# Performance work log

Measured on AMD Instinct MI355X. Metric: run time of the kernel, lower is better.

## Reference

```python
import jax, jax.numpy as jnp
import numpy as np

N_IN = 1024
N_OUT = 1024
N_SAMPLES = 64
BATCH = 4096
SIGMA_INITIAL = 0.1
MUMAX_INITIAL = 1.0


def setup_inputs() -> dict:
    key = jax.random.key(0)
    ks = jax.random.split(key, 5)
    lsig = jnp.float32(np.log(SIGMA_INITIAL))
    return {
        "x": jax.random.normal(ks[0], (BATCH, N_IN), dtype=jnp.float32),
        "w_mu": jax.random.uniform(ks[1], (N_OUT, N_IN), dtype=jnp.float32,
                                   minval=-MUMAX_INITIAL, maxval=MUMAX_INITIAL),
        "w_lsigma": jnp.full((N_OUT, N_IN), lsig, dtype=jnp.float32),
        "b_mu": jax.random.uniform(ks[2], (N_OUT,), dtype=jnp.float32,
                                   minval=-MUMAX_INITIAL, maxval=MUMAX_INITIAL),
        "b_lsigma": jnp.full((N_OUT,), lsig, dtype=jnp.float32),
        "r1": jax.random.normal(ks[3], (N_SAMPLES, N_OUT, N_IN), dtype=jnp.float32),
        "r2": jax.random.normal(ks[4], (N_SAMPLES, N_OUT), dtype=jnp.float32),
        "N_samples": N_SAMPLES,
    }


def reference(x, w_mu, w_lsigma, b_mu, b_lsigma, r1, r2, N_samples):
    # Reparameterized weight/bias samples: (S, N_out, N_in), (S, N_out)
    w = w_mu + jnp.exp(w_lsigma) * r1
    b = b_mu + jnp.exp(b_lsigma) * r2
    # y[s, b, o] = sum_i x[b, i] * w[s, o, i] + b[s, o]
    y = jnp.einsum('bi,soi->sbo', x, w) + b[:, None, :]
    return y
```

## Files before the change

### kernel.cpp

```cpp
#include <hip/hip_runtime.h>
#include <hip/hip_bf16.h>
#include <hip/hip_fp8.h>
#include <stdint.h>
#include <type_traits>

#define NIN  1024
#define NOUT 1024
#define NB   4096

typedef float f32x4  __attribute__((ext_vector_type(4)));
typedef float f32x16 __attribute__((ext_vector_type(16)));
typedef __bf16 bf16x8 __attribute__((ext_vector_type(8)));
typedef int   i32x4 __attribute__((ext_vector_type(4)));
typedef int   i32x8 __attribute__((ext_vector_type(8)));

typedef const __attribute__((address_space(1))) unsigned int* gp1_t;
typedef __attribute__((address_space(3))) unsigned int* lp3_t;

__device__ __forceinline__ void gload16(const void* g, void* l) {
    __builtin_amdgcn_global_load_lds((gp1_t)g, (lp3_t)l, 16, 0, 0);
}

__device__ __forceinline__ unsigned short f2bf(float f) {
    __bf16 h = (__bf16)f;
    return __builtin_bit_cast(unsigned short, h);
}

__device__ __forceinline__ unsigned int pk4_fp8(float a, float b, float c, float d) {
#if __has_builtin(__builtin_amdgcn_cvt_pk_fp8_f32)
    int p = __builtin_amdgcn_cvt_pk_fp8_f32(a, b, 0, false);
    p = __builtin_amdgcn_cvt_pk_fp8_f32(c, d, p, true);
    return (unsigned int)p;
#else
    __hip_fp8_e4m3 qa(a), qb(b), qc(c), qd(d);
    return (unsigned int)qa.__x | ((unsigned int)qb.__x << 8) |
           ((unsigned int)qc.__x << 16) | ((unsigned int)qd.__x << 24);
#endif
}

#define BAR   __builtin_amdgcn_s_barrier()
#define LGK0  do { asm volatile("s_waitcnt lgkmcnt(0)" ::: "memory"); __builtin_amdgcn_sched_barrier(0); } while (0)
#define VMW2  do { asm volatile("s_waitcnt vmcnt(2)"  ::: "memory"); __builtin_amdgcn_sched_barrier(0); } while (0)
#define VMW0  do { asm volatile("s_waitcnt vmcnt(0)"  ::: "memory"); __builtin_amdgcn_sched_barrier(0); } while (0)

__global__ void cvt_x_kernel(const float* __restrict__ x, unsigned short* __restrict__ xb) {
    int i = blockIdx.x * blockDim.x + threadIdx.x;
    f32x4 v = reinterpret_cast<const f32x4*>(x)[i];
    ushort4 o;
    o.x = f2bf(v.x); o.y = f2bf(v.y); o.z = f2bf(v.z); o.w = f2bf(v.w);
    reinterpret_cast<ushort4*>(xb)[i] = o;
}

__global__ void cvt_x_fp8(const float* __restrict__ x, unsigned int* __restrict__ xf8) {
    int i = blockIdx.x * blockDim.x + threadIdx.x;
    f32x4 v = reinterpret_cast<const f32x4*>(x)[i];
    xf8[i] = pk4_fp8(v.x, v.y, v.z, v.w);
}

__global__ void cvt_r1_fp8(const float* __restrict__ wls, const float* __restrict__ r1,
                           unsigned int* __restrict__ rf8, int s0) {
    int idx = blockIdx.x * blockDim.x + threadIdx.x;
    int i4 = idx & 262143;
    int c  = idx >> 18;
    f32x4 ls = reinterpret_cast<const f32x4*>(wls)[i4];
    const f32x4* rp = reinterpret_cast<const f32x4*>(r1 + ((size_t)(s0 + c) << 20));
    f32x4 r = __builtin_nontemporal_load(rp + i4);
    rf8[idx] = pk4_fp8(__expf(ls.x) * r.x, __expf(ls.y) * r.y,
                       __expf(ls.z) * r.z, __expf(ls.w) * r.w);
}

__global__ void bias_kernel(const float* __restrict__ bmu, const float* __restrict__ bls,
                            const float* __restrict__ r2, float* __restrict__ bias, int total) {
    int i = blockIdx.x * blockDim.x + threadIdx.x;
    if (i < total) {
        int o = i & (NOUT - 1);
        bias[i] = bmu[o] + __expf(bls[o]) * r2[i];
    }
}

__launch_bounds__(512, 2)
__global__ void gemm256(const unsigned short* __restrict__ xb,
                        const unsigned short* __restrict__ wb,
                        float* __restrict__ out, int nwg) {
    __shared__ __align__(16) char smem[131072];
    const int tid = threadIdx.x;
    const int l   = tid & 63;
    const int w   = tid >> 6;
    const int wr  = w >> 2, wc = w & 3;

    const int b   = blockIdx.x;
    const int q8  = nwg >> 3;
    const int g   = (b & 7) * q8 + (b >> 3);
    const int mi  = g & 15;
    const int ni  = g >> 4;
    const int m0  = mi * 256;
    const int n0  = ni * 256;

    const int srow = l >> 3;
    const int scol = ((l & 7) ^ srow) * 8;
    const size_t slane = (size_t)srow * NIN + scol;

    const int rowp  = (l & 15) * 128;
    const int colp0 = ((l >> 4) ^ (l & 7)) << 4;

    f32x4 acc[8][4] = {};
    bf16x8 aF[4][2], b0F[2][2], b1F[2][2];

    const unsigned short* xbase = xb + (size_t)m0 * NIN;
    const unsigned short* wbase = wb + (size_t)n0 * NIN;

    auto STAGE = [&](int buf, int kt, int q) {
        const int R = (q & 3) * 64 + w * 8;
        const unsigned short* src = ((q < 4) ? xbase : wbase)
                                    + (size_t)R * NIN + kt * 64 + slane;
        char* dst = smem + buf * 65536 + ((q >= 4) ? 32768 : 0) + R * 128;
        gload16(src, dst);
    };
    auto LDA = [&](int buf, int mh) {
        const char* base = smem + buf * 65536 + (wr * 128 + mh * 64) * 128 + rowp;
        #pragma unroll
        for (int mb = 0; mb < 4; ++mb) {
            aF[mb][0] = *(const bf16x8*)(base + mb * 2048 + colp0);
            aF[mb][1] = *(const bf16x8*)(base + mb * 2048 + (colp0 ^ 64));
        }
    };
    auto LDB = [&](bf16x8 (&bF)[2][2], int buf, int nh) {
        const char* base = smem + buf * 65536 + 32768 + (wc * 64 + nh * 32) * 128 + rowp;
        #pragma unroll
        for (int nb = 0; nb < 2; ++nb) {
            bF[nb][0] = *(const bf16x8*)(base + nb * 2048 + colp0);
            bF[nb][1] = *(const bf16x8*)(base + nb * 2048 + (colp0 ^ 64));
        }
    };
    auto MM = [&](auto MHc, auto NHc, bf16x8 (&bF)[2][2]) {
        constexpr int MH = decltype(MHc)::value;
        constexpr int NH = decltype(NHc)::value;
        __builtin_amdgcn_s_setprio(1);
        #pragma unroll
        for (int mb = 0; mb < 4; ++mb)
            #pragma unroll
            for (int nb = 0; nb < 2; ++nb)
                #pragma unroll
                for (int kk = 0; kk < 2; ++kk)
                    acc[MH * 4 + mb][NH * 2 + nb] = __builtin_amdgcn_mfma_f32_16x16x32_bf16(
                        aF[mb][kk], bF[nb][kk], acc[MH * 4 + mb][NH * 2 + nb], 0, 0, 0);
        __builtin_amdgcn_s_setprio(0);
    };

    auto C0 = std::integral_constant<int, 0>{};
    auto C1 = std::integral_constant<int, 1>{};

    auto ITER = [&](auto LASTc, int t1, int t2, int t3) {
        constexpr bool LAST = decltype(LASTc)::value;
        LDA(0, 0); LDB(b0F, 0, 0);
        STAGE(1, t1, 2); STAGE(1, t1, 3);
        BAR; LGK0; MM(C0, C0, b0F); BAR;
        LDB(b1F, 0, 1);
        STAGE(1, t1, 4); STAGE(1, t1, 5);
        BAR; LGK0; MM(C0, C1, b1F); BAR;
        LDA(0, 1);
        STAGE(1, t1, 6); STAGE(1, t1, 7);
        BAR; LGK0; MM(C1, C1, b1F); BAR;
        if constexpr (!LAST) { STAGE(0, t2, 0); STAGE(0, t2, 1); }
        BAR; MM(C1, C0, b0F);
        if constexpr (LAST) { VMW0; } else { VMW2; }
        BAR;
        LDA(1, 0); LDB(b0F, 1, 0);
        if constexpr (!LAST) { STAGE(0, t2, 2); STAGE(0, t2, 3); }
        BAR; LGK0; MM(C0, C0, b0F); BAR;
        LDB(b1F, 1, 1);
        if constexpr (!LAST) { STAGE(0, t2, 4); STAGE(0, t2, 5); }
        BAR; LGK0; MM(C0, C1, b1F); BAR;
        LDA(1, 1);
        if constexpr (!LAST) { STAGE(0, t2, 6); STAGE(0, t2, 7); }
        BAR; LGK0; MM(C1, C1, b1F); BAR;
        if constexpr (!LAST) {
            STAGE(1, t3, 0); STAGE(1, t3, 1);
            BAR; MM(C1, C0, b0F); VMW2; BAR;
        } else {
            MM(C1, C0, b0F);
        }
    };

    #pragma unroll
    for (int q = 0; q < 8; ++q) STAGE(0, 0, q);
    STAGE(1, 1, 0); STAGE(1, 1, 1);
    VMW2; BAR;

    #pragma unroll 1
    for (int i = 0; i < 7; ++i)
        ITER(std::false_type{}, 2 * i + 1, 2 * i + 2, 2 * i + 3);
    ITER(std::true_type{}, 15, 16, 17);

    const int oc = n0 + wc * 64 + (l & 15);
    float* outp = out;
    #pragma unroll
    for (int mb = 0; mb < 8; ++mb) {
        #pragma unroll
        for (int i2 = 0; i2 < 4; ++i2) {
            int row = m0 + wr * 128 + mb * 16 + (l >> 4) * 4 + i2;
            float* rp = outp + (size_t)row * NOUT + oc;
            #pragma unroll
            for (int nb = 0; nb < 4; ++nb)
                rp[nb * 16] = acc[mb][nb][i2];
        }
    }
}

__launch_bounds__(512, 2)
__global__ void gemm256mx(const unsigned char* __restrict__ xf8,
                          const unsigned char* __restrict__ rf8,
                          const float* __restrict__ y0,
                          const float* __restrict__ bias,
                          float* __restrict__ out, int s0, int nwg) {
    __shared__ __align__(16) char smem[131072];
    const int tid = threadIdx.x;
    const int l   = tid & 63;
    const int w   = tid >> 6;
    const int wr  = w >> 2, wc = w & 3;

    const int b   = blockIdx.x;
    const int q8  = nwg >> 3;
    const int g   = (b & 7) * q8 + (b >> 3);
    const int mi  = g & 15;
    const int ni  = g >> 4;
    const int m0  = mi * 256;
    const int n0  = ni * 256;

    const int srow  = l >> 3;
    const int scolb = ((l & 7) ^ srow) * 16;
    const size_t slane = (size_t)srow * NIN + scolb;

    const int arow = l & 31;
    const int swz  = l & 7;
    const int kgrp = (l >> 5) * 2;

    f32x16 acc[4][2] = {};
    i32x8 aF[2][2], b0F[2], b1F[2];

    const unsigned char* xbase = xf8 + (size_t)m0 * NIN;
    const unsigned char* rbase = rf8 + (size_t)n0 * NIN;

    auto STAGE = [&](int buf, int kt, int q) {
        const int R = (q & 3) * 64 + w * 8;
        const unsigned char* src = ((q < 4) ? xbase : rbase)
                                   + (size_t)R * NIN + kt * 128 + slane;
        char* dst = smem + buf * 65536 + ((q >= 4) ? 32768 : 0) + R * 128;
        gload16(src, dst);
    };

    auto LDA = [&](int buf, int mh) {
        const char* base = smem + buf * 65536 + (wr * 128 + mh * 64 + arow) * 128;
        #pragma unroll
        for (int mb = 0; mb < 2; ++mb) {
            const char* rb = base + mb * 4096;
            #pragma unroll
            for (int ks = 0; ks < 2; ++ks) {
                int c = ks * 4 + kgrp;
                i32x4 lo = *(const i32x4*)(rb + ((c ^ swz) * 16));
                i32x4 hi = *(const i32x4*)(rb + (((c + 1) ^ swz) * 16));
                aF[mb][ks] = __builtin_shufflevector(lo, hi, 0, 1, 2, 3, 4, 5, 6, 7);
            }
        }
    };
    auto LDB = [&](i32x8 (&bF)[2], int buf, int nh) {
        const char* base = smem + buf * 65536 + 32768 + (wc * 64 + nh * 32 + arow) * 128;
        #pragma unroll
        for (int ks = 0; ks < 2; ++ks) {
            int c = ks * 4 + kgrp;
            i32x4 lo = *(const i32x4*)(base + ((c ^ swz) * 16));
            i32x4 hi = *(const i32x4*)(base + (((c + 1) ^ swz) * 16));
            bF[ks] = __builtin_shufflevector(lo, hi, 0, 1, 2, 3, 4, 5, 6, 7);
        }
    };

    auto MM = [&](auto MHc, auto NHc, i32x8 (&bF)[2]) {
        constexpr int MH = decltype(MHc)::value;
        constexpr int NH = decltype(NHc)::value;
        __builtin_amdgcn_s_setprio(1);
        #pragma unroll
        for (int mb = 0; mb < 2; ++mb)
            #pragma unroll
            for (int ks = 0; ks < 2; ++ks)
                acc[MH * 2 + mb][NH] = __builtin_amdgcn_mfma_scale_f32_32x32x64_f8f6f4(
                    aF[mb][ks], bF[ks], acc[MH * 2 + mb][NH],
                    0, 0,
                    0, 127,
                    0, 127);
        __builtin_amdgcn_s_setprio(0);
    };

    auto C0 = std::integral_constant<int, 0>{};
    auto C1 = std::integral_constant<int, 1>{};

    auto ITER = [&](auto LASTc, int t1, int t2, int t3) {
        constexpr bool LAST = decltype(LASTc)::value;
        LDA(0, 0); LDB(b0F, 0, 0);
        STAGE(1, t1, 2); STAGE(1, t1, 3);
        BAR; LGK0; MM(C0, C0, b0F); BAR;
        LDB(b1F, 0, 1);
        STAGE(1, t1, 4); STAGE(1, t1, 5);
        BAR; LGK0; MM(C0, C1, b1F); BAR;
        LDA(0, 1);
        STAGE(1, t1, 6); STAGE(1, t1, 7);
        BAR; LGK0; MM(C1, C1, b1F); BAR;
        if constexpr (!LAST) { STAGE(0, t2, 0); STAGE(0, t2, 1); }
        BAR; MM(C1, C0, b0F);
        if constexpr (LAST) { VMW0; } else { VMW2; }
        BAR;
        LDA(1, 0); LDB(b0F, 1, 0);
        if constexpr (!LAST) { STAGE(0, t2, 2); STAGE(0, t2, 3); }
        BAR; LGK0; MM(C0, C0, b0F); BAR;
        LDB(b1F, 1, 1);
        if constexpr (!LAST) { STAGE(0, t2, 4); STAGE(0, t2, 5); }
        BAR; LGK0; MM(C0, C1, b1F); BAR;
        LDA(1, 1);
        if constexpr (!LAST) { STAGE(0, t2, 6); STAGE(0, t2, 7); }
        BAR; LGK0; MM(C1, C1, b1F); BAR;
        if constexpr (!LAST) {
            STAGE(1, t3, 0); STAGE(1, t3, 1);
            BAR; MM(C1, C0, b0F); VMW2; BAR;
        } else {
            MM(C1, C0, b0F);
        }
    };

    #pragma unroll
    for (int q = 0; q < 8; ++q) STAGE(0, 0, q);
    STAGE(1, 1, 0); STAGE(1, 1, 1);
    VMW2; BAR;

    #pragma unroll 1
    for (int i = 0; i < 3; ++i)
        ITER(std::false_type{}, 2 * i + 1, 2 * i + 2, 2 * i + 3);
    ITER(std::true_type{}, 7, 8, 9);

    const int s   = s0 + (n0 >> 10);
    const int n0c = n0 & 1023;
    float* outp = out + (size_t)s * NB * NOUT;
    float* lds_f = (float*)smem;
    const f32x4 bvv = *(const f32x4*)(bias + (size_t)s * NOUT + n0c + l * 4);

    #pragma unroll
    for (int c = 0; c < 4; ++c) {
        if (wr == (c >> 1)) {
            #pragma unroll
            for (int mbh = 0; mbh < 2; ++mbh) {
                const int mb = (c & 1) * 2 + mbh;
                #pragma unroll
                for (int nb = 0; nb < 2; ++nb) {
                    const int col = wc * 64 + nb * 32 + (l & 31);
                    #pragma unroll
                    for (int r = 0; r < 16; ++r) {
                        int rl = mbh * 32 + 4 * (l >> 5) + (r & 3) + 8 * (r >> 2);
                        lds_f[rl * 256 + col] = acc[mb][nb][r];
                    }
                }
            }
        }
        LGK0; BAR;
        #pragma unroll
        for (int k = 0; k < 8; ++k) {
            const int rl  = k * 8 + w;
            const int row = m0 + c * 64 + rl;
            f32x4 v  = *(const f32x4*)(lds_f + (rl * 64 + l) * 4);
            f32x4 yv = *(const f32x4*)(y0 + (size_t)row * NOUT + n0c + l * 4);
            f32x4 o  = v + yv + bvv;
            __builtin_nontemporal_store(o, (f32x4*)(outp + (size_t)row * NOUT + n0c + l * 4));
        }
        BAR;
    }
}

__global__ void fused_fallback(const float* __restrict__ x, const float* __restrict__ wmu,
                               const float* __restrict__ wls, const float* __restrict__ r1,
                               const float* __restrict__ bmu, const float* __restrict__ bls,
                               const float* __restrict__ r2, float* __restrict__ out) {
    __shared__ float Xs[16][64];
    __shared__ float Ws[16][64];
    int b0 = blockIdx.x * 16, o0 = blockIdx.y * 16, s = blockIdx.z;
    int tb = threadIdx.x >> 4, to = threadIdx.x & 15;
    float acc = 0.f;
    for (int k0 = 0; k0 < NIN; k0 += 64) {
        __syncthreads();
        #pragma unroll
        for (int j = 0; j < 4; ++j) {
            int e = j * 256 + threadIdx.x;
            int r = e >> 6, cc = e & 63;
            Xs[r][cc] = x[(size_t)(b0 + r) * NIN + k0 + cc];
            size_t wi = (size_t)(o0 + r) * NIN + k0 + cc;
            Ws[r][cc] = wmu[wi] + __expf(wls[wi]) * r1[(size_t)s * NIN * NOUT + wi];
        }
        __syncthreads();
        for (int k = 0; k < 64; ++k) acc += Xs[tb][k] * Ws[to][k];
    }
    int o = o0 + to;
    out[((size_t)s * NB + b0 + tb) * NOUT + o] = acc + bmu[o] + __expf(bls[o]) * r2[s * NOUT + o];
}

extern "C" void kernel_launch(void* const* d_in, const int* in_sizes, int n_in,
                              void* d_out, int out_size, void* d_ws, size_t ws_size,
                              hipStream_t stream) {
    const float* x   = (const float*)d_in[0];
    const float* wmu = (const float*)d_in[1];
    const float* wls = (const float*)d_in[2];
    const float* bmu = (const float*)d_in[3];
    const float* bls = (const float*)d_in[4];
    const float* r1  = (const float*)d_in[5];
    const float* r2  = (const float*)d_in[6];
    const int S = in_sizes[6] / NOUT;
    float* out = (float*)d_out;

    const size_t xb_b   = (size_t)NB * NIN * 2;
    const size_t xf8_b  = (size_t)NB * NIN;
    const size_t wmub_b = (size_t)NOUT * NIN * 2;
    const size_t y0_b   = (size_t)NB * NOUT * 4;
    const size_t bias_b = (size_t)S * NOUT * 4;
    const size_t per_s  = (size_t)NOUT * NIN;
    const size_t base_b = xb_b + xf8_b + wmub_b + y0_b + bias_b;

    if (ws_size < base_b + per_s) {
        dim3 gg(NB / 16, NOUT / 16, S);
        fused_fallback<<<gg, 256, 0, stream>>>(x, wmu, wls, r1, bmu, bls, r2, out);
        return;
    }

    char* ws = (char*)d_ws;
    unsigned short* xb   = (unsigned short*)ws;
    unsigned char*  xf8  = (unsigned char*)(ws + xb_b);
    unsigned short* wmub = (unsigned short*)(ws + xb_b + xf8_b);
    float*          y0   = (float*)(ws + xb_b + xf8_b + wmub_b);
    float*          bias = (float*)(ws + xb_b + xf8_b + wmub_b + y0_b);
    unsigned char*  rf8  = (unsigned char*)(ws + base_b);

    int SC = (int)((ws_size - base_b) / per_s);
    if (SC > S) SC = S;

    cvt_x_kernel<<<NB * NIN / 1024, 256, 0, stream>>>(x, xb);
    cvt_x_kernel<<<NOUT * NIN / 1024, 256, 0, stream>>>(wmu, wmub);
    cvt_x_fp8<<<NB * NIN / 1024, 256, 0, stream>>>(x, (unsigned int*)xf8);
    bias_kernel<<<(S * NOUT + 255) / 256, 256, 0, stream>>>(bmu, bls, r2, bias, S * NOUT);

    gemm256<<<64, 512, 0, stream>>>(xb, wmub, y0, 64);

    for (int s0 = 0; s0 < S; s0 += SC) {
        int sc = (S - s0 < SC) ? (S - s0) : SC;
        cvt_r1_fp8<<<sc * (NOUT * NIN / 1024), 256, 0, stream>>>(wls, r1, (unsigned int*)rf8, s0);
        int nwg = 64 * sc;
        gemm256mx<<<nwg, 512, 0, stream>>>(xf8, rf8, y0, bias, out, s0, nwg);
    }
}
```

Baseline: 643.8 us.

## Prefetch whole k-tiles at once instead of interleaving loads with MFMA phases

The main GEMM loop now issues all eight global-to-LDS loads for the next k-tile of a buffer in one batch (STAGE8), rather than spreading them across the MFMA sub-phases. The vmcnt waits change from 2 to 8 to match. Block-to-tile mapping also changes from a fixed 16-row modulo to a division based on nwg. This gives each tile a longer prefetch lead, in exchange for burstier memory traffic and possible clustering of loads against the LDS buffer still being read.

```diff
diff --git a/kernel.cpp b/kernel.cpp
--- a/kernel.cpp
+++ b/kernel.cpp
@@ -40,6 +40,7 @@
 
 #define BAR   __builtin_amdgcn_s_barrier()
 #define LGK0  do { asm volatile("s_waitcnt lgkmcnt(0)" ::: "memory"); __builtin_amdgcn_sched_barrier(0); } while (0)
+#define VMW8  do { asm volatile("s_waitcnt vmcnt(8)"  ::: "memory"); __builtin_amdgcn_sched_barrier(0); } while (0)
 #define VMW2  do { asm volatile("s_waitcnt vmcnt(2)"  ::: "memory"); __builtin_amdgcn_sched_barrier(0); } while (0)
 #define VMW0  do { asm volatile("s_waitcnt vmcnt(0)"  ::: "memory"); __builtin_amdgcn_sched_barrier(0); } while (0)
 
@@ -222,8 +223,9 @@
     const int b   = blockIdx.x;
     const int q8  = nwg >> 3;
     const int g   = (b & 7) * q8 + (b >> 3);
-    const int mi  = g & 15;
-    const int ni  = g >> 4;
+    const int nni = nwg >> 4;
+    const int mi  = g / nni;
+    const int ni  = g - mi * nni;
     const int m0  = mi * 256;
     const int n0  = ni * 256;
 
@@ -247,6 +249,10 @@
                                    + (size_t)R * NIN + kt * 128 + slane;
         char* dst = smem + buf * 65536 + ((q >= 4) ? 32768 : 0) + R * 128;
         gload16(src, dst);
+    };
+    auto STAGE8 = [&](int buf, int kt) {
+        #pragma unroll
+        for (int q = 0; q < 8; ++q) STAGE(buf, kt, q);
     };
 
     auto LDA = [&](int buf, int mh) {
@@ -293,47 +299,40 @@
     auto C0 = std::integral_constant<int, 0>{};
     auto C1 = std::integral_constant<int, 1>{};
 
-    auto ITER = [&](auto LASTc, int t1, int t2, int t3) {
+    auto ITER = [&](auto LASTc, int t2, int t3) {
         constexpr bool LAST = decltype(LASTc)::value;
         LDA(0, 0); LDB(b0F, 0, 0);
-        STAGE(1, t1, 2); STAGE(1, t1, 3);
         BAR; LGK0; MM(C0, C0, b0F); BAR;
         LDB(b1F, 0, 1);
-        STAGE(1, t1, 4); STAGE(1, t1, 5);
         BAR; LGK0; MM(C0, C1, b1F); BAR;
         LDA(0, 1);
-        STAGE(1, t1, 6); STAGE(1, t1, 7);
         BAR; LGK0; MM(C1, C1, b1F); BAR;
-        if constexpr (!LAST) { STAGE(0, t2, 0); STAGE(0, t2, 1); }
+        if constexpr (!LAST) STAGE8(0, t2);
         BAR; MM(C1, C0, b0F);
-        if constexpr (LAST) { VMW0; } else { VMW2; }
+        if constexpr (LAST) { VMW0; } else { VMW8; }
         BAR;
         LDA(1, 0); LDB(b0F, 1, 0);
-        if constexpr (!LAST) { STAGE(0, t2, 2); STAGE(0, t2, 3); }
         BAR; LGK0; MM(C0, C0, b0F); BAR;
         LDB(b1F, 1, 1);
-        if constexpr (!LAST) { STAGE(0, t2, 4); STAGE(0, t2, 5); }
         BAR; LGK0; MM(C0, C1, b1F); BAR;
         LDA(1, 1);
-        if constexpr (!LAST) { STAGE(0, t2, 6); STAGE(0, t2, 7); }
         BAR; LGK0; MM(C1, C1, b1F); BAR;
         if constexpr (!LAST) {
-            STAGE(1, t3, 0); STAGE(1, t3, 1);
-            BAR; MM(C1, C0, b0F); VMW2; BAR;
+            STAGE8(1, t3);
+            BAR; MM(C1, C0, b0F); VMW8; BAR;
         } else {
             MM(C1, C0, b0F);
         }
     };
 
-    #pragma unroll
-    for (int q = 0; q < 8; ++q) STAGE(0, 0, q);
-    STAGE(1, 1, 0); STAGE(1, 1, 1);
-    VMW2; BAR;
+    STAGE8(0, 0);
+    STAGE8(1, 1);
+    VMW8; BAR;
 
     #pragma unroll 1
     for (int i = 0; i < 3; ++i)
-        ITER(std::false_type{}, 2 * i + 1, 2 * i + 2, 2 * i + 3);
-    ITER(std::true_type{}, 7, 8, 9);
+        ITER(std::false_type{}, 2 * i + 2, 2 * i + 3);
+    ITER(std::true_type{}, 8, 9);
 
     const int s   = s0 + (n0 >> 10);
     const int n0c = n0 & 1023;
```

New measurement: 561.5 us. 1.15x faster.
